# Kernel tuning notes

Hardware: AMD Instinct MI355X
Metric: run time of the kernel (lower is better)

The kernel has to match this reference:

```python
import jax, jax.numpy as jnp
import numpy as np

B, C_IN, C_OUT, H, W, K = 8, 32, 32, 96, 96, 5


def setup_inputs() -> dict:
    key = jax.random.key(0)
    k1, k2 = jax.random.split(key)
    f = jax.random.normal(k1, (B, C_IN, H, W), dtype=jnp.float32)
    # xavier_uniform-style init for the structuring element h
    fan_in = C_IN * K * K
    fan_out = C_OUT * K * K
    bound = float(np.sqrt(6.0 / (fan_in + fan_out)))
    h = jax.random.uniform(k2, (C_OUT, C_IN, K, K), dtype=jnp.float32,
                           minval=-bound, maxval=bound)
    return {"f": f, "h": h}


def reference(f, h):
    """Morphological max-plus dilation with 'same' padding.

    out[b,o,y,x] = max_{c,i,j} f[b,c,y+i-p, x+j-p] + h[o,c,i,j]
    """
    b, c, hh, ww = f.shape
    o, _, k, _ = h.shape
    p = k // 2
    neg = -jnp.finfo(f.dtype).max / 2
    fp = jnp.pad(f, ((0, 0), (0, 0), (p, p), (p, p)), constant_values=neg)
    out = jnp.full((b, o, hh, ww), neg, dtype=f.dtype)
    for i in range(k):          # fixed small kernel loop (k*k = 25 taps)
        for j in range(k):
            sl = fp[:, :, i:i + hh, j:j + ww]              # (B, C, H, W)
            w_ij = h[:, :, i, j]                            # (O, C)
            # max-plus over input channels: (B,1,C,H,W) + (O,C,1,1)
            cand = jnp.max(sl[:, None] + w_ij[None, :, :, None, None], axis=2)
            out = jnp.maximum(out, cand)
    return out
```

## Files before the change

kernel.cpp:

```cpp
#include <hip/hip_runtime.h>


#define B_ 8
#define C_ 32
#define O_ 32
#define H_ 96
#define W_ 96
#define K_ 5
#define KK_ (K_ * K_)
#define NCP_ (C_ / 2)

#define TX_ 24
#define RT_ 8
#define CS_ 2
#define TY_ (RT_ * CS_)
#define NT_ (TX_ * TY_)
#define XR_ 4
#define OB_ 4
#define CPG_ (NCP_ / CS_)

#define PH_ 100
#define PW_ 104
#define PLSZ_ (PH_ * PW_)
#define FPAD_BYTES ((size_t)B_ * NCP_ * PLSZ_ * 4)

#define HBLK_ 128
#define HPACK_DW (8 * NCP_ * HBLK_)

#define NEGF (-30000.0f)

typedef _Float16 h2 __attribute__((ext_vector_type(2)));
typedef int sv8 __attribute__((ext_vector_type(8)));
typedef int sv4 __attribute__((ext_vector_type(4)));

static __device__ __forceinline__ h2 h2b(unsigned u) {
    return __builtin_bit_cast(h2, u);
}
static __device__ __forceinline__ unsigned bh2(h2 v) {
    return __builtin_bit_cast(unsigned, v);
}

static __device__ __forceinline__ void pk_addmax_s(h2& acc, h2 fv, int hs) {
    h2 t;
    asm("v_pk_add_f16 %0, %1, %2" : "=v"(t) : "v"(fv), "s"(hs));
    asm("v_pk_max_f16 %0, %1, %2" : "=v"(acc) : "v"(acc), "v"(t));
}

static __device__ __forceinline__ int hgetA(sv8 a0, sv8 a1, sv8 a2, sv8 a3,
                                            sv8 a4, sv8 a5, int n) {
    if (n < 8)  return a0[n];
    if (n < 16) return a1[n - 8];
    if (n < 24) return a2[n - 16];
    if (n < 32) return a3[n - 24];
    if (n < 40) return a4[n - 32];
    return a5[n - 40];
}
static __device__ __forceinline__ int hgetB(sv8 a0, sv8 a1, sv8 a2, sv8 a3,
                                            sv8 a4, sv8 a5, sv4 b, int n) {
    if (n < 48) return hgetA(a0, a1, a2, a3, a4, a5, n);
    return b[n - 48];
}

__global__ __launch_bounds__(256)
void prepad_kernel(const float* __restrict__ f, unsigned* __restrict__ fpad) {
    const int idx = blockIdx.x * 256 + threadIdx.x;
    const int cp = blockIdx.y;
    const int b  = blockIdx.z;
    if (idx >= PLSZ_) return;
    const int row = idx / PW_;
    const int col = idx - row * PW_;
    const int y = row - 2;
    const int x = col - 2;
    float v0 = NEGF, v1 = NEGF;
    if ((unsigned)y < H_ && (unsigned)x < W_) {
        v0 = f[((size_t)(b * C_ + 2 * cp)     * H_ + y) * W_ + x];
        v1 = f[((size_t)(b * C_ + 2 * cp + 1) * H_ + y) * W_ + x];
    }
    h2 d; d.x = (_Float16)v0; d.y = (_Float16)v1;
    fpad[(size_t)(b * NCP_ + cp) * PLSZ_ + idx] = bh2(d);
}

__global__ __launch_bounds__(256)
void hpack_kernel(const float* __restrict__ h, unsigned* __restrict__ hpack) {
    const int idx = blockIdx.x * 256 + threadIdx.x;
    if (idx >= 8 * NCP_ * KK_ * OB_) return;
    const int og = idx / (NCP_ * KK_ * OB_);
    int r  = idx - og * (NCP_ * KK_ * OB_);
    const int cp = r / (KK_ * OB_);
    r -= cp * (KK_ * OB_);
    const int ij = r / OB_;
    const int o  = r - ij * OB_;
    float a0 = h[((size_t)(og * OB_ + o) * C_ + 2 * cp)     * KK_ + ij];
    float a1 = h[((size_t)(og * OB_ + o) * C_ + 2 * cp + 1) * KK_ + ij];
    h2 p; p.x = (_Float16)a0; p.y = (_Float16)a1;
    hpack[(size_t)(og * NCP_ + cp) * HBLK_ + ij * OB_ + o] = bh2(p);
}

__global__ __launch_bounds__(NT_)
void dilate_main(const unsigned* __restrict__ fpad,
                 const unsigned* __restrict__ hpack,
                 float* __restrict__ out) {
    const int tx  = threadIdx.x;
    const int ty  = threadIdx.y;
    const int ry  = ty & (RT_ - 1);
    const int g   = ty >> 3;
    const int gu  = __builtin_amdgcn_readfirstlane(g);

    const int ytile = blockIdx.x;
    const int og    = blockIdx.y;
    const int b     = blockIdx.z;
    const int y0 = ytile * RT_;
    const int o0 = og * OB_;
    const int x0 = XR_ * tx;
    const int yb = y0 + ry;

    __shared__ unsigned short comb[OB_ * XR_][RT_ * TX_];

    h2 acc[OB_][XR_];
    {
        h2 neg; neg.x = (_Float16)NEGF; neg.y = (_Float16)NEGF;
#pragma unroll
        for (int o = 0; o < OB_; ++o)
#pragma unroll
            for (int xx = 0; xx < XR_; ++xx) acc[o][xx] = neg;
    }

    const int cp0v = g * CPG_;
    const int cp0s = gu * CPG_;
    for (int cpi = 0; cpi < CPG_; ++cpi) {
        h2 win[K_][8];
        {
            const unsigned* p = fpad +
                (size_t)(b * NCP_ + cp0v + cpi) * PLSZ_ + yb * PW_ + x0;
#pragma unroll
            for (int i = 0; i < K_; ++i) {
                const uint4* q = (const uint4*)(p + i * PW_);
                uint4 w0 = q[0];
                uint4 w1 = q[1];
                win[i][0] = h2b(w0.x); win[i][1] = h2b(w0.y);
                win[i][2] = h2b(w0.z); win[i][3] = h2b(w0.w);
                win[i][4] = h2b(w1.x); win[i][5] = h2b(w1.y);
                win[i][6] = h2b(w1.z); win[i][7] = h2b(w1.w);
            }
        }

        const unsigned* hp =
            hpack + (size_t)(og * NCP_ + cp0s + cpi) * HBLK_;

        sv8 a0, a1, a2, a3, a4, a5;
        asm volatile(
            "s_load_dwordx8 %0, %6, 0x0\n\t"
            "s_load_dwordx8 %1, %6, 0x20\n\t"
            "s_load_dwordx8 %2, %6, 0x40\n\t"
            "s_load_dwordx8 %3, %6, 0x60\n\t"
            "s_load_dwordx8 %4, %6, 0x80\n\t"
            "s_load_dwordx8 %5, %6, 0xa0\n\t"
            "s_waitcnt lgkmcnt(0)"
            : "=s"(a0), "=s"(a1), "=s"(a2), "=s"(a3), "=s"(a4), "=s"(a5)
            : "s"(hp));

#pragma unroll
        for (int ij = 0; ij < 12; ++ij) {
            const int i = ij / K_, j = ij % K_;
            const int n = ij * 4;
            int h0 = hgetA(a0, a1, a2, a3, a4, a5, n);
            int h1 = hgetA(a0, a1, a2, a3, a4, a5, n + 1);
            int h2v = hgetA(a0, a1, a2, a3, a4, a5, n + 2);
            int h3 = hgetA(a0, a1, a2, a3, a4, a5, n + 3);
#pragma unroll
            for (int xx = 0; xx < XR_; ++xx) {
                h2 fv = win[i][xx + j];
                pk_addmax_s(acc[0][xx], fv, h0);
                pk_addmax_s(acc[1][xx], fv, h1);
                pk_addmax_s(acc[2][xx], fv, h2v);
                pk_addmax_s(acc[3][xx], fv, h3);
            }
        }

        sv8 b0, b1, b2, b3, b4, b5;
        sv4 bt;
        asm volatile(
            "s_load_dwordx8 %0, %7, 0xc0\n\t"
            "s_load_dwordx8 %1, %7, 0xe0\n\t"
            "s_load_dwordx8 %2, %7, 0x100\n\t"
            "s_load_dwordx8 %3, %7, 0x120\n\t"
            "s_load_dwordx8 %4, %7, 0x140\n\t"
            "s_load_dwordx8 %5, %7, 0x160\n\t"
            "s_load_dwordx4 %6, %7, 0x180\n\t"
            "s_waitcnt lgkmcnt(0)"
            : "=s"(b0), "=s"(b1), "=s"(b2), "=s"(b3), "=s"(b4), "=s"(b5),
              "=s"(bt)
            : "s"(hp));

#pragma unroll
        for (int ij = 12; ij < KK_; ++ij) {
            const int i = ij / K_, j = ij % K_;
            const int n = ij * 4 - 48;
            int h0 = hgetB(b0, b1, b2, b3, b4, b5, bt, n);
            int h1 = hgetB(b0, b1, b2, b3, b4, b5, bt, n + 1);
            int h2v = hgetB(b0, b1, b2, b3, b4, b5, bt, n + 2);
            int h3 = hgetB(b0, b1, b2, b3, b4, b5, bt, n + 3);
#pragma unroll
            for (int xx = 0; xx < XR_; ++xx) {
                h2 fv = win[i][xx + j];
                pk_addmax_s(acc[0][xx], fv, h0);
                pk_addmax_s(acc[1][xx], fv, h1);
                pk_addmax_s(acc[2][xx], fv, h2v);
                pk_addmax_s(acc[3][xx], fv, h3);
            }
        }
    }

    unsigned short red[OB_][XR_];
#pragma unroll
    for (int o = 0; o < OB_; ++o)
#pragma unroll
        for (int xx = 0; xx < XR_; ++xx) {
            _Float16 a = acc[o][xx].x;
            _Float16 b2 = acc[o][xx].y;
            _Float16 m = (a > b2) ? a : b2;
            red[o][xx] = __builtin_bit_cast(unsigned short, m);
        }

    const int t192 = ry * TX_ + tx;
    if (g == 1) {
#pragma unroll
        for (int o = 0; o < OB_; ++o)
#pragma unroll
            for (int xx = 0; xx < XR_; ++xx)
                comb[o * XR_ + xx][t192] = red[o][xx];
    }
    __syncthreads();
    if (g == 0) {
        const int y = yb;
#pragma unroll
        for (int o = 0; o < OB_; ++o) {
            float r[XR_];
#pragma unroll
            for (int xx = 0; xx < XR_; ++xx) {
                _Float16 m  = __builtin_bit_cast(_Float16, red[o][xx]);
                _Float16 v0 = __builtin_bit_cast(_Float16,
                                                 comb[o * XR_ + xx][t192]);
                m = (v0 > m) ? v0 : m;
                r[xx] = (float)m;
            }
            float4 v = make_float4(r[0], r[1], r[2], r[3]);
            *(float4*)&out[(((size_t)b * O_ + (o0 + o)) * H_ + y) * W_ + x0] = v;
        }
    }
}

__global__ __launch_bounds__(256)
void dilate_naive(const float* __restrict__ f, const float* __restrict__ h,
                  float* __restrict__ out) {
    const int idx = blockIdx.x * 256 + threadIdx.x;
    if (idx >= B_ * O_ * H_ * W_) return;
    const int x = idx % W_;
    const int y = (idx / W_) % H_;
    const int o = (idx / (W_ * H_)) % O_;
    const int b = idx / (W_ * H_ * O_);
    float m = -3.0e38f;
    for (int c = 0; c < C_; ++c)
        for (int i = 0; i < K_; ++i)
            for (int j = 0; j < K_; ++j) {
                int yy = y + i - 2, xc = x + j - 2;
                if ((unsigned)yy < H_ && (unsigned)xc < W_) {
                    float v = f[((size_t)(b * C_ + c) * H_ + yy) * W_ + xc] +
                              h[((size_t)o * C_ + c) * KK_ + i * K_ + j];
                    m = fmaxf(m, v);
                }
            }
    out[idx] = m;
}

extern "C" void kernel_launch(void* const* d_in, const int* in_sizes, int n_in,
                              void* d_out, int out_size, void* d_ws, size_t ws_size,
                              hipStream_t stream) {
    const float* f = (const float*)d_in[0];
    const float* h = (const float*)d_in[1];
    float* out = (float*)d_out;

    const size_t need = FPAD_BYTES + (size_t)HPACK_DW * 4;
    if (ws_size >= need) {
        unsigned* fpad  = (unsigned*)d_ws;
        unsigned* hpack = (unsigned*)((char*)d_ws + FPAD_BYTES);
        dim3 pgrid((PLSZ_ + 255) / 256, NCP_, B_);
        hipLaunchKernelGGL(prepad_kernel, pgrid, dim3(256), 0, stream, f, fpad);
        hipLaunchKernelGGL(hpack_kernel,
                           dim3((8 * NCP_ * KK_ * OB_ + 255) / 256), dim3(256),
                           0, stream, h, hpack);
        dim3 mgrid(H_ / RT_, O_ / OB_, B_);
        dim3 mblock(TX_, TY_);
        hipLaunchKernelGGL(dilate_main, mgrid, mblock, 0, stream,
                           fpad, hpack, out);
    } else {
        hipLaunchKernelGGL(dilate_naive,
                           dim3((B_ * O_ * H_ * W_ + 255) / 256), dim3(256),
                           0, stream, f, h, out);
    }
}
```

Measured before the change: 139.4 us.

## Software-pipeline window and weight loads per kernel row, merge prep kernels

The main dilation loop now works in per-row phases. Each phase prefetches the next row's window with inline global loads and the next row's scalar weights with s_load into double-buffered registers, using explicit waitcnt. This replaces bulk loading of the whole 5-row window and 25 taps before compute. The packed weight layout is reorganised to 24 dwords per kernel row to match. The prepad and hpack kernels are fused into a single launch to save a dispatch. The hand-written asm waitcnt scheme is fragile and relies on exact counts of outstanding loads.

```diff
diff --git a/kernel.cpp b/kernel.cpp
--- a/kernel.cpp
+++ b/kernel.cpp
@@ -25,6 +25,7 @@
 #define FPAD_BYTES ((size_t)B_ * NCP_ * PLSZ_ * 4)
 
 #define HBLK_ 128
+#define HPH_ 24
 #define HPACK_DW (8 * NCP_ * HBLK_)
 
 #define NEGF (-30000.0f)
@@ -32,6 +33,7 @@
 typedef _Float16 h2 __attribute__((ext_vector_type(2)));
 typedef int sv8 __attribute__((ext_vector_type(8)));
 typedef int sv4 __attribute__((ext_vector_type(4)));
+typedef unsigned uv4 __attribute__((ext_vector_type(4)));
 
 static __device__ __forceinline__ h2 h2b(unsigned u) {
     return __builtin_bit_cast(h2, u);
@@ -46,54 +48,100 @@
     asm("v_pk_max_f16 %0, %1, %2" : "=v"(acc) : "v"(acc), "v"(t));
 }
 
-static __device__ __forceinline__ int hgetA(sv8 a0, sv8 a1, sv8 a2, sv8 a3,
-                                            sv8 a4, sv8 a5, int n) {
-    if (n < 8)  return a0[n];
-    if (n < 16) return a1[n - 8];
-    if (n < 24) return a2[n - 16];
-    if (n < 32) return a3[n - 24];
-    if (n < 40) return a4[n - 32];
-    return a5[n - 40];
-}
-static __device__ __forceinline__ int hgetB(sv8 a0, sv8 a1, sv8 a2, sv8 a3,
-                                            sv8 a4, sv8 a5, sv4 b, int n) {
-    if (n < 48) return hgetA(a0, a1, a2, a3, a4, a5, n);
-    return b[n - 48];
-}
+static __device__ __forceinline__ int hget20(sv8 a, sv8 b, sv4 c, int n) {
+    if (n < 8)  return a[n];
+    if (n < 16) return b[n - 8];
+    return c[n - 16];
+}
+
+static __device__ __forceinline__ h2 getwin(uv4 a, uv4 b, int d) {
+    if (d == 0) return h2b(a[0]);
+    if (d == 1) return h2b(a[1]);
+    if (d == 2) return h2b(a[2]);
+    if (d == 3) return h2b(a[3]);
+    if (d == 4) return h2b(b[0]);
+    if (d == 5) return h2b(b[1]);
+    if (d == 6) return h2b(b[2]);
+    return h2b(b[3]);
+}
+
+static __device__ __forceinline__ void compute_phase(h2 (&acc)[OB_][XR_],
+        uv4 wa, uv4 wb, sv8 c0, sv8 c1, sv4 c2) {
+#pragma unroll
+    for (int j = 0; j < K_; ++j) {
+        const int n = j * 4;
+        const int h0 = hget20(c0, c1, c2, n);
+        const int h1 = hget20(c0, c1, c2, n + 1);
+        const int h2v = hget20(c0, c1, c2, n + 2);
+        const int h3 = hget20(c0, c1, c2, n + 3);
+#pragma unroll
+        for (int xx = 0; xx < XR_; ++xx) {
+            h2 fv = getwin(wa, wb, xx + j);
+            pk_addmax_s(acc[0][xx], fv, h0);
+            pk_addmax_s(acc[1][xx], fv, h1);
+            pk_addmax_s(acc[2][xx], fv, h2v);
+            pk_addmax_s(acc[3][xx], fv, h3);
+        }
+    }
+}
+
+#define HLOADM(B0, B1, B2, HP, O0S, O1S, O2S)                          \
+    asm volatile("s_load_dwordx8 %0, %3, " O0S "\n\t"                  \
+                 "s_load_dwordx8 %1, %3, " O1S "\n\t"                  \
+                 "s_load_dwordx4 %2, %3, " O2S                         \
+                 : "=s"(B0), "=s"(B1), "=s"(B2) : "s"(HP))
+
+#define WLOADM(SA, SB, PTR)                                            \
+    asm volatile("global_load_dwordx4 %0, %2, off\n\t"                 \
+                 "global_load_dwordx4 %1, %2, off offset:16"           \
+                 : "=v"(SA), "=v"(SB) : "v"(PTR))
+
+#define PHASE(CB0, CB1, CB2, NB0, NB1, NB2, NHP, O0S, O1S, O2S, WS, PS, PPTR) \
+    do {                                                                      \
+        asm volatile("s_waitcnt lgkmcnt(0)"                                   \
+                     : "+s"(CB0), "+s"(CB1), "+s"(CB2));                      \
+        HLOADM(NB0, NB1, NB2, NHP, O0S, O1S, O2S);                            \
+        asm volatile("s_waitcnt vmcnt(6)"                                     \
+                     : "+v"(win[WS][0]), "+v"(win[WS][1]));                   \
+        WLOADM(win[PS][0], win[PS][1], PPTR);                                 \
+        compute_phase(acc, win[WS][0], win[WS][1], CB0, CB1, CB2);            \
+    } while (0)
 
 __global__ __launch_bounds__(256)
-void prepad_kernel(const float* __restrict__ f, unsigned* __restrict__ fpad) {
-    const int idx = blockIdx.x * 256 + threadIdx.x;
-    const int cp = blockIdx.y;
-    const int b  = blockIdx.z;
-    if (idx >= PLSZ_) return;
-    const int row = idx / PW_;
-    const int col = idx - row * PW_;
-    const int y = row - 2;
-    const int x = col - 2;
-    float v0 = NEGF, v1 = NEGF;
-    if ((unsigned)y < H_ && (unsigned)x < W_) {
-        v0 = f[((size_t)(b * C_ + 2 * cp)     * H_ + y) * W_ + x];
-        v1 = f[((size_t)(b * C_ + 2 * cp + 1) * H_ + y) * W_ + x];
-    }
-    h2 d; d.x = (_Float16)v0; d.y = (_Float16)v1;
-    fpad[(size_t)(b * NCP_ + cp) * PLSZ_ + idx] = bh2(d);
-}
-
-__global__ __launch_bounds__(256)
-void hpack_kernel(const float* __restrict__ h, unsigned* __restrict__ hpack) {
-    const int idx = blockIdx.x * 256 + threadIdx.x;
-    if (idx >= 8 * NCP_ * KK_ * OB_) return;
-    const int og = idx / (NCP_ * KK_ * OB_);
-    int r  = idx - og * (NCP_ * KK_ * OB_);
-    const int cp = r / (KK_ * OB_);
-    r -= cp * (KK_ * OB_);
-    const int ij = r / OB_;
-    const int o  = r - ij * OB_;
-    float a0 = h[((size_t)(og * OB_ + o) * C_ + 2 * cp)     * KK_ + ij];
-    float a1 = h[((size_t)(og * OB_ + o) * C_ + 2 * cp + 1) * KK_ + ij];
-    h2 p; p.x = (_Float16)a0; p.y = (_Float16)a1;
-    hpack[(size_t)(og * NCP_ + cp) * HBLK_ + ij * OB_ + o] = bh2(p);
+void prep_kernel(const float* __restrict__ f, const float* __restrict__ h,
+                 unsigned* __restrict__ fpad, unsigned* __restrict__ hpack) {
+    const int bz = blockIdx.z;
+    if (bz < B_) {
+        const int idx = blockIdx.x * 256 + threadIdx.x;
+        const int cp = blockIdx.y;
+        if (idx >= PLSZ_) return;
+        const int row = idx / PW_;
+        const int col = idx - row * PW_;
+        const int y = row - 2;
+        const int x = col - 2;
+        float v0 = NEGF, v1 = NEGF;
+        if ((unsigned)y < H_ && (unsigned)x < W_) {
+            v0 = f[((size_t)(bz * C_ + 2 * cp)     * H_ + y) * W_ + x];
+            v1 = f[((size_t)(bz * C_ + 2 * cp + 1) * H_ + y) * W_ + x];
+        }
+        h2 d; d.x = (_Float16)v0; d.y = (_Float16)v1;
+        fpad[(size_t)(bz * NCP_ + cp) * PLSZ_ + idx] = bh2(d);
+    } else {
+        const int t = (blockIdx.y * gridDim.x + blockIdx.x) * 256 + threadIdx.x;
+        if (t >= 8 * NCP_ * KK_ * OB_) return;
+        const int og = t / (NCP_ * KK_ * OB_);
+        int r  = t - og * (NCP_ * KK_ * OB_);
+        const int cp = r / (KK_ * OB_);
+        r -= cp * (KK_ * OB_);
+        const int ij = r / OB_;
+        const int o  = r - ij * OB_;
+        const int p  = ij / K_;
+        const int jj = ij - p * K_;
+        float a0 = h[((size_t)(og * OB_ + o) * C_ + 2 * cp)     * KK_ + ij];
+        float a1 = h[((size_t)(og * OB_ + o) * C_ + 2 * cp + 1) * KK_ + ij];
+        h2 pv; pv.x = (_Float16)a0; pv.y = (_Float16)a1;
+        hpack[(size_t)(og * NCP_ + cp) * HBLK_ + p * HPH_ + jj * 4 + o] = bh2(pv);
+    }
 }
 
 __global__ __launch_bounds__(NT_)
@@ -127,89 +175,46 @@
 
     const int cp0v = g * CPG_;
     const int cp0s = gu * CPG_;
-    for (int cpi = 0; cpi < CPG_; ++cpi) {
-        h2 win[K_][8];
-        {
-            const unsigned* p = fpad +
-                (size_t)(b * NCP_ + cp0v + cpi) * PLSZ_ + yb * PW_ + x0;
-#pragma unroll
-            for (int i = 0; i < K_; ++i) {
-                const uint4* q = (const uint4*)(p + i * PW_);
-                uint4 w0 = q[0];
-                uint4 w1 = q[1];
-                win[i][0] = h2b(w0.x); win[i][1] = h2b(w0.y);
-                win[i][2] = h2b(w0.z); win[i][3] = h2b(w0.w);
-                win[i][4] = h2b(w1.x); win[i][5] = h2b(w1.y);
-                win[i][6] = h2b(w1.z); win[i][7] = h2b(w1.w);
-            }
-        }
-
-        const unsigned* hp =
-            hpack + (size_t)(og * NCP_ + cp0s + cpi) * HBLK_;
-
-        sv8 a0, a1, a2, a3, a4, a5;
-        asm volatile(
-            "s_load_dwordx8 %0, %6, 0x0\n\t"
-            "s_load_dwordx8 %1, %6, 0x20\n\t"
-            "s_load_dwordx8 %2, %6, 0x40\n\t"
-            "s_load_dwordx8 %3, %6, 0x60\n\t"
-            "s_load_dwordx8 %4, %6, 0x80\n\t"
-            "s_load_dwordx8 %5, %6, 0xa0\n\t"
-            "s_waitcnt lgkmcnt(0)"
-            : "=s"(a0), "=s"(a1), "=s"(a2), "=s"(a3), "=s"(a4), "=s"(a5)
-            : "s"(hp));
-
-#pragma unroll
-        for (int ij = 0; ij < 12; ++ij) {
-            const int i = ij / K_, j = ij % K_;
-            const int n = ij * 4;
-            int h0 = hgetA(a0, a1, a2, a3, a4, a5, n);
-            int h1 = hgetA(a0, a1, a2, a3, a4, a5, n + 1);
-            int h2v = hgetA(a0, a1, a2, a3, a4, a5, n + 2);
-            int h3 = hgetA(a0, a1, a2, a3, a4, a5, n + 3);
-#pragma unroll
-            for (int xx = 0; xx < XR_; ++xx) {
-                h2 fv = win[i][xx + j];
-                pk_addmax_s(acc[0][xx], fv, h0);
-                pk_addmax_s(acc[1][xx], fv, h1);
-                pk_addmax_s(acc[2][xx], fv, h2v);
-                pk_addmax_s(acc[3][xx], fv, h3);
-            }
-        }
-
-        sv8 b0, b1, b2, b3, b4, b5;
-        sv4 bt;
-        asm volatile(
-            "s_load_dwordx8 %0, %7, 0xc0\n\t"
-            "s_load_dwordx8 %1, %7, 0xe0\n\t"
-            "s_load_dwordx8 %2, %7, 0x100\n\t"
-            "s_load_dwordx8 %3, %7, 0x120\n\t"
-            "s_load_dwordx8 %4, %7, 0x140\n\t"
-            "s_load_dwordx8 %5, %7, 0x160\n\t"
-            "s_load_dwordx4 %6, %7, 0x180\n\t"
-            "s_waitcnt lgkmcnt(0)"
-            : "=s"(b0), "=s"(b1), "=s"(b2), "=s"(b3), "=s"(b4), "=s"(b5),
-              "=s"(bt)
-            : "s"(hp));
-
-#pragma unroll
-        for (int ij = 12; ij < KK_; ++ij) {
-            const int i = ij / K_, j = ij % K_;
-            const int n = ij * 4 - 48;
-            int h0 = hgetB(b0, b1, b2, b3, b4, b5, bt, n);
-            int h1 = hgetB(b0, b1, b2, b3, b4, b5, bt, n + 1);
-            int h2v = hgetB(b0, b1, b2, b3, b4, b5, bt, n + 2);
-            int h3 = hgetB(b0, b1, b2, b3, b4, b5, bt, n + 3);
-#pragma unroll
-            for (int xx = 0; xx < XR_; ++xx) {
-                h2 fv = win[i][xx + j];
-                pk_addmax_s(acc[0][xx], fv, h0);
-                pk_addmax_s(acc[1][xx], fv, h1);
-                pk_addmax_s(acc[2][xx], fv, h2v);
-                pk_addmax_s(acc[3][xx], fv, h3);
-            }
-        }
-    }
+    const unsigned* hpb = hpack + (size_t)(og * NCP_ + cp0s) * HBLK_;
+    const unsigned* pvb = fpad + (size_t)(b * NCP_ + cp0v) * PLSZ_ + yb * PW_ + x0;
+
+    sv8 hA0, hA1; sv4 hA2;
+    sv8 hB0, hB1; sv4 hB2;
+    uv4 win[5][2];
+
+    HLOADM(hA0, hA1, hA2, hpb, "0x0", "0x20", "0x40");
+    WLOADM(win[0][0], win[0][1], pvb);
+    WLOADM(win[1][0], win[1][1], pvb + PW_);
+    WLOADM(win[2][0], win[2][1], pvb + 2 * PW_);
+    WLOADM(win[3][0], win[3][1], pvb + 3 * PW_);
+
+#pragma unroll 1
+    for (int cpi = 0; cpi < CPG_; cpi += 2) {
+        const unsigned* hb0 = hpb + (size_t)cpi * HBLK_;
+        const unsigned* hb1 = hb0 + HBLK_;
+        const unsigned* hb2 = (cpi + 2 < CPG_) ? hb1 + HBLK_ : hb1;
+        const unsigned* pv0 = pvb + (size_t)cpi * PLSZ_;
+        const unsigned* pv1 = pv0 + PLSZ_;
+        const unsigned* pv2 = (cpi + 2 < CPG_) ? pv1 + PLSZ_ : pv1;
+
+        PHASE(hA0,hA1,hA2, hB0,hB1,hB2, hb0, "0x60","0x80","0xa0",   0, 4, pv0 + 4*PW_);
+        PHASE(hB0,hB1,hB2, hA0,hA1,hA2, hb0, "0xc0","0xe0","0x100",  1, 0, pv1);
+        PHASE(hA0,hA1,hA2, hB0,hB1,hB2, hb0, "0x120","0x140","0x160",2, 1, pv1 + PW_);
+        PHASE(hB0,hB1,hB2, hA0,hA1,hA2, hb0, "0x180","0x1a0","0x1c0",3, 2, pv1 + 2*PW_);
+        PHASE(hA0,hA1,hA2, hB0,hB1,hB2, hb1, "0x0","0x20","0x40",    4, 3, pv1 + 3*PW_);
+        PHASE(hB0,hB1,hB2, hA0,hA1,hA2, hb1, "0x60","0x80","0xa0",   0, 4, pv1 + 4*PW_);
+        PHASE(hA0,hA1,hA2, hB0,hB1,hB2, hb1, "0xc0","0xe0","0x100",  1, 0, pv2);
+        PHASE(hB0,hB1,hB2, hA0,hA1,hA2, hb1, "0x120","0x140","0x160",2, 1, pv2 + PW_);
+        PHASE(hA0,hA1,hA2, hB0,hB1,hB2, hb1, "0x180","0x1a0","0x1c0",3, 2, pv2 + 2*PW_);
+        PHASE(hB0,hB1,hB2, hA0,hA1,hA2, hb2, "0x0","0x20","0x40",    4, 3, pv2 + 3*PW_);
+    }
+
+    asm volatile("s_waitcnt vmcnt(0) lgkmcnt(0)"
+                 : "+v"(win[0][0]), "+v"(win[0][1]),
+                   "+v"(win[1][0]), "+v"(win[1][1]),
+                   "+v"(win[2][0]), "+v"(win[2][1]),
+                   "+v"(win[3][0]), "+v"(win[3][1]),
+                   "+s"(hA0), "+s"(hA1), "+s"(hA2));
 
     unsigned short red[OB_][XR_];
 #pragma unroll
@@ -284,11 +289,9 @@
     if (ws_size >= need) {
         unsigned* fpad  = (unsigned*)d_ws;
         unsigned* hpack = (unsigned*)((char*)d_ws + FPAD_BYTES);
-        dim3 pgrid((PLSZ_ + 255) / 256, NCP_, B_);
-        hipLaunchKernelGGL(prepad_kernel, pgrid, dim3(256), 0, stream, f, fpad);
-        hipLaunchKernelGGL(hpack_kernel,
-                           dim3((8 * NCP_ * KK_ * OB_ + 255) / 256), dim3(256),
-                           0, stream, h, hpack);
+        dim3 pgrid((PLSZ_ + 255) / 256, NCP_, B_ + 1);
+        hipLaunchKernelGGL(prep_kernel, pgrid, dim3(256), 0, stream,
+                           f, h, fpad, hpack);
         dim3 mgrid(H_ / RT_, O_ / OB_, B_);
         dim3 mblock(TX_, TY_);
         hipLaunchKernelGGL(dilate_main, mgrid, mblock, 0, stream,
```

After: 139.5 us. No clear change (+0.0%).
